# Kernel optimization log

Hardware: AMD Instinct MI355X
Metric: run time of the kernel (lower is better)

Reference implementation:

```python
import jax, jax.numpy as jnp
import numpy as np

N_SEG = 128  # number of distinct batch ids (patients/samples)
N = 250000   # total cells
E = 128      # embed_dim
H = 4        # num_heads

def setup_inputs() -> dict:
    key = jax.random.key(0)
    k1, k2, k3 = jax.random.split(key, 3)
    x = jax.random.normal(k1, (N, E), dtype=jnp.float32)
    weights = jax.random.normal(k2, (H, E), dtype=jnp.float32) * 0.02
    batch = jnp.sort(jax.random.randint(k3, (N,), 0, N_SEG, dtype=jnp.int64))
    return {"x": x, "weights": weights, "batch": batch}

def reference(x, weights, batch):
    # att[n,h] = <x[n], weights[h]>
    att = x @ weights.T  # [N, H]
    # segment-wise (per batch id) stable softmax over the sample axis
    m = jax.lax.stop_gradient(jax.ops.segment_max(att, batch, num_segments=N_SEG))  # [N_SEG, H]
    e = jnp.exp(att - m[batch])                                                     # [N, H]
    s = jax.ops.segment_sum(e, batch, num_segments=N_SEG)                           # [N_SEG, H]
    att_sm = e / s[batch]                                                           # [N, H]
    # h[b, h, e] = sum_{n in segment b} att_sm[n, h] * x[n, e]
    h = jax.ops.segment_sum(att_sm[:, :, None] * x[:, None, :], batch, num_segments=N_SEG)  # [N_SEG, H, E]
    # cat=False -> average over heads
    return h.mean(axis=1)  # [N_SEG, E]
```

## Files before the change

kernel.cpp:

```cpp
#include <hip/hip_runtime.h>

#define EDIM 128
#define NHEAD 4
#define NSEG 128
#define LOG2E 1.4426950408889634f

typedef float f32x8 __attribute__((ext_vector_type(8)));


#define DOT8(xv, wv)                                                     \
    fmaf((xv)[7], (wv)[7], fmaf((xv)[6], (wv)[6],                        \
    fmaf((xv)[5], (wv)[5], fmaf((xv)[4], (wv)[4],                        \
    fmaf((xv)[3], (wv)[3], fmaf((xv)[2], (wv)[2],                        \
    fmaf((xv)[1], (wv)[1], (xv)[0] * (wv)[0])))))))

#define RED16(v) do { v += __shfl_xor(v, 1, 64); v += __shfl_xor(v, 2, 64); \
                      v += __shfl_xor(v, 4, 64); v += __shfl_xor(v, 8, 64); } while (0)
#define REDG(v)  do { v += __shfl_xor(v, 16, 64); v += __shfl_xor(v, 32, 64); } while (0)

#define FLUSH_STORE(seg) do {                                            \
    float t0 = s0, t1 = s1, t2 = s2, t3 = s3;                            \
    REDG(t0); REDG(t1); REDG(t2); REDG(t3);                              \
    f32x8 r0 = a0, r1 = a1, r2 = a2, r3 = a3;                            \
    _Pragma("unroll")                                                    \
    for (int j = 0; j < 8; ++j) {                                        \
        float u0 = r0[j]; REDG(u0); r0[j] = u0;                          \
        float u1 = r1[j]; REDG(u1); r1[j] = u1;                          \
        float u2 = r2[j]; REDG(u2); r2[j] = u2;                          \
        float u3 = r3[j]; REDG(u3); r3[j] = u3;                          \
    }                                                                    \
    f32x8 rv = (g == 0) ? r0 : ((g == 1) ? r1 : ((g == 2) ? r2 : r3));   \
    const size_t ent_ = (size_t)wave * 2 + (nflushed < 1 ? 0 : 1);       \
    *reinterpret_cast<f32x8*>(pouth + ent_ * 512 + g * EDIM + 8 * c) = rv; \
    if (lane == 0) {                                                     \
        psum[ent_ * 4 + 0] = t0; psum[ent_ * 4 + 1] = t1;                \
        psum[ent_ * 4 + 2] = t2; psum[ent_ * 4 + 3] = t3;                \
        pseg[ent_] = (seg);                                              \
    }                                                                    \
    nflushed++;                                                          \
    a0 = Z8; a1 = Z8; a2 = Z8; a3 = Z8;                                  \
    s0 = 0.f; s1 = 0.f; s2 = 0.f; s3 = 0.f;                              \
} while (0)

__global__ __launch_bounds__(256) void attn_agg_pass1(
    const float* __restrict__ x, const float* __restrict__ w,
    const int* __restrict__ batch,
    float* __restrict__ pouth,
    float* __restrict__ psum,
    int*   __restrict__ pseg,
    int n, int qpw)
{
    const int tid  = blockIdx.x * blockDim.x + threadIdx.x;
    const int wave = tid >> 6;
    const int lane = threadIdx.x & 63;
    const int g    = lane >> 4;
    const int c    = lane & 15;

    const int nquads = (n + 3) >> 2;
    const int q0 = wave * qpw;
    if (q0 >= nquads) {
        if (lane == 0) { pseg[(size_t)wave * 2] = -1; pseg[(size_t)wave * 2 + 1] = -1; }
        return;
    }
    const int q1 = min(q0 + qpw, nquads);

    const float* wp = w + 8 * c;
    const f32x8 w0 = *reinterpret_cast<const f32x8*>(wp + 0 * EDIM);
    const f32x8 w1 = *reinterpret_cast<const f32x8*>(wp + 1 * EDIM);
    const f32x8 w2 = *reinterpret_cast<const f32x8*>(wp + 2 * EDIM);
    const f32x8 w3 = *reinterpret_cast<const f32x8*>(wp + 3 * EDIM);

    const f32x8 Z8 = {0.f, 0.f, 0.f, 0.f, 0.f, 0.f, 0.f, 0.f};
    f32x8 a0 = Z8, a1 = Z8, a2 = Z8, a3 = Z8;
    float s0 = 0.f, s1 = 0.f, s2 = 0.f, s3 = 0.f;
    int nflushed = 0;

    int cur_b = __builtin_amdgcn_readfirstlane(batch[q0 * 4]);

    for (int q = q0; q < q1; ++q) {
        const int cell = q * 4 + g;
        const int row  = min(cell, n - 1);
        const f32x8 xv = *reinterpret_cast<const f32x8*>(
            x + (size_t)row * EDIM + 8 * c);

        float p0 = DOT8(xv, w0);
        float p1 = DOT8(xv, w1);
        float p2 = DOT8(xv, w2);
        float p3 = DOT8(xv, w3);
        RED16(p0); RED16(p1); RED16(p2); RED16(p3);

        const float e0 = __builtin_exp2f(p0 * LOG2E);
        const float e1 = __builtin_exp2f(p1 * LOG2E);
        const float e2 = __builtin_exp2f(p2 * LOG2E);
        const float e3 = __builtin_exp2f(p3 * LOG2E);

        const bool full = (q * 4 + 3 < n);
        const int  b3   = __builtin_amdgcn_readfirstlane(batch[min(q * 4 + 3, n - 1)]);

        if (full && b3 == cur_b) {
            s0 += e0; s1 += e1; s2 += e2; s3 += e3;
            a0 += xv * e0; a1 += xv * e1; a2 += xv * e2; a3 += xv * e3;
        } else {
            const int my_b = (cell < n) ? batch[cell] : -2;
            const bool m1 = (my_b == cur_b);
            const float f1 = m1 ? 1.f : 0.f;
            s0 += e0 * f1; s1 += e1 * f1; s2 += e2 * f1; s3 += e3 * f1;
            a0 += xv * (e0 * f1); a1 += xv * (e1 * f1);
            a2 += xv * (e2 * f1); a3 += xv * (e3 * f1);

            FLUSH_STORE(cur_b);
            cur_b = b3;

            const float f2 = (!m1 && my_b == cur_b) ? 1.f : 0.f;
            s0 += e0 * f2; s1 += e1 * f2; s2 += e2 * f2; s3 += e3 * f2;
            a0 += xv * (e0 * f2); a1 += xv * (e1 * f2);
            a2 += xv * (e2 * f2); a3 += xv * (e3 * f2);
        }
    }

    FLUSH_STORE(cur_b);
    if (lane == 0 && nflushed < 2) pseg[(size_t)wave * 2 + 1] = -1;
}

__global__ __launch_bounds__(512) void attn_agg_finish(
    const float* __restrict__ pouth, const float* __restrict__ psum,
    const int* __restrict__ pseg, float* __restrict__ out, int nent)
{
    const int b = blockIdx.x;
    const int t = threadIdx.x;
    const int h = t >> 7, d = t & (EDIM - 1);

    __shared__ int matches[512];
    __shared__ int nmatch;
    __shared__ float hacc[NHEAD][EDIM];
    if (t == 0) nmatch = 0;
    __syncthreads();

    for (int i = t; i < nent; i += 512) {
        if (pseg[i] == b) {
            int p = atomicAdd(&nmatch, 1);
            matches[p] = i;
        }
    }
    __syncthreads();

    float acc = 0.f, sh = 0.f;
    const int nm = nmatch;
    for (int k = 0; k < nm; ++k) {
        const int i = matches[k];
        acc += pouth[(size_t)i * 512 + t];
        sh  += psum[(size_t)i * 4 + h];
    }
    hacc[h][d] = (sh > 0.f) ? (acc / sh) : 0.f;
    __syncthreads();

    if (h == 0)
        out[b * EDIM + d] = 0.25f *
            (hacc[0][d] + hacc[1][d] + hacc[2][d] + hacc[3][d]);
}

extern "C" void kernel_launch(void* const* d_in, const int* in_sizes, int n_in,
                              void* d_out, int out_size, void* d_ws, size_t ws_size,
                              hipStream_t stream) {
    const float* x     = (const float*)d_in[0];
    const float* w     = (const float*)d_in[1];
    const int*   batch = (const int*)d_in[2];
    float* out = (float*)d_out;

    const int n = in_sizes[0] / EDIM;
    const int nquads = (n + 3) >> 2;

    const size_t per_wave = 2 * (512 * 4 + 4 * 4 + 4);
    int W = (int)(ws_size / per_wave) - 4;
    if (W > 4096) W = 4096;
    if (W < 64)   W = 64;
    W &= ~3;

    const int qpw      = (nquads + W - 1) / W;
    const int nw       = (nquads + qpw - 1) / qpw;
    const int blocks1  = (nw + 3) / 4;
    const int launched = blocks1 * 4;
    const int nent     = launched * 2;

    float* pouth = (float*)d_ws;
    float* psum  = pouth + (size_t)nent * 512;
    int*   pseg  = (int*)(psum + (size_t)nent * 4);

    attn_agg_pass1<<<blocks1, 256, 0, stream>>>(x, w, batch, pouth, psum, pseg, n, qpw);
    attn_agg_finish<<<NSEG, 512, 0, stream>>>(pouth, psum, pseg, out, nent);
}
```

Baseline: 202.9 us.

## Add single-segment fast path, DPP reductions, and double wave count

Adds a fast path for waves whose whole cell range lies in one segment, which skips the per-quad batch loads and boundary checks and walks x with an incrementing pointer. The 16-lane dot-product reductions now use DPP row operations instead of shuffles. The wave cap rises from 4096 to 8192, so each wave handles fewer quads and occupancy improves. The finish kernel's match buffer is enlarged and clamped to fit the extra partial entries. The cost is more partial results for the finish kernel to scan and reduce.

```diff
diff --git a/kernel.cpp b/kernel.cpp
--- a/kernel.cpp
+++ b/kernel.cpp
@@ -14,8 +14,18 @@
     fmaf((xv)[3], (wv)[3], fmaf((xv)[2], (wv)[2],                        \
     fmaf((xv)[1], (wv)[1], (xv)[0] * (wv)[0])))))))
 
-#define RED16(v) do { v += __shfl_xor(v, 1, 64); v += __shfl_xor(v, 2, 64); \
-                      v += __shfl_xor(v, 4, 64); v += __shfl_xor(v, 8, 64); } while (0)
+__device__ __forceinline__ float dpp_add16(float v) {
+    v += __int_as_float(__builtin_amdgcn_update_dpp(
+        0, __float_as_int(v), 0xB1, 0xF, 0xF, true));
+    v += __int_as_float(__builtin_amdgcn_update_dpp(
+        0, __float_as_int(v), 0x4E, 0xF, 0xF, true));
+    v += __int_as_float(__builtin_amdgcn_update_dpp(
+        0, __float_as_int(v), 0x124, 0xF, 0xF, true));
+    v += __int_as_float(__builtin_amdgcn_update_dpp(
+        0, __float_as_int(v), 0x128, 0xF, 0xF, true));
+    return v;
+}
+
 #define REDG(v)  do { v += __shfl_xor(v, 16, 64); v += __shfl_xor(v, 32, 64); } while (0)
 
 #define FLUSH_STORE(seg) do {                                            \
@@ -75,46 +85,72 @@
     float s0 = 0.f, s1 = 0.f, s2 = 0.f, s3 = 0.f;
     int nflushed = 0;
 
+    const int cellN = min(q1 * 4, n);
     int cur_b = __builtin_amdgcn_readfirstlane(batch[q0 * 4]);
-
-    for (int q = q0; q < q1; ++q) {
-        const int cell = q * 4 + g;
-        const int row  = min(cell, n - 1);
-        const f32x8 xv = *reinterpret_cast<const f32x8*>(
-            x + (size_t)row * EDIM + 8 * c);
-
-        float p0 = DOT8(xv, w0);
-        float p1 = DOT8(xv, w1);
-        float p2 = DOT8(xv, w2);
-        float p3 = DOT8(xv, w3);
-        RED16(p0); RED16(p1); RED16(p2); RED16(p3);
-
-        const float e0 = __builtin_exp2f(p0 * LOG2E);
-        const float e1 = __builtin_exp2f(p1 * LOG2E);
-        const float e2 = __builtin_exp2f(p2 * LOG2E);
-        const float e3 = __builtin_exp2f(p3 * LOG2E);
-
-        const bool full = (q * 4 + 3 < n);
-        const int  b3   = __builtin_amdgcn_readfirstlane(batch[min(q * 4 + 3, n - 1)]);
-
-        if (full && b3 == cur_b) {
+    const int last_b = __builtin_amdgcn_readfirstlane(batch[cellN - 1]);
+
+    if (cur_b == last_b && q1 * 4 <= n) {
+        const float* xp = x + (size_t)(q0 * 4 + g) * EDIM + 8 * c;
+        for (int q = q0; q < q1; ++q) {
+            const f32x8 xv = *reinterpret_cast<const f32x8*>(xp);
+            xp += 4 * EDIM;
+
+            float p0 = DOT8(xv, w0);
+            float p1 = DOT8(xv, w1);
+            float p2 = DOT8(xv, w2);
+            float p3 = DOT8(xv, w3);
+            p0 = dpp_add16(p0); p1 = dpp_add16(p1);
+            p2 = dpp_add16(p2); p3 = dpp_add16(p3);
+
+            const float e0 = __builtin_exp2f(p0 * LOG2E);
+            const float e1 = __builtin_exp2f(p1 * LOG2E);
+            const float e2 = __builtin_exp2f(p2 * LOG2E);
+            const float e3 = __builtin_exp2f(p3 * LOG2E);
+
             s0 += e0; s1 += e1; s2 += e2; s3 += e3;
             a0 += xv * e0; a1 += xv * e1; a2 += xv * e2; a3 += xv * e3;
-        } else {
-            const int my_b = (cell < n) ? batch[cell] : -2;
-            const bool m1 = (my_b == cur_b);
-            const float f1 = m1 ? 1.f : 0.f;
-            s0 += e0 * f1; s1 += e1 * f1; s2 += e2 * f1; s3 += e3 * f1;
-            a0 += xv * (e0 * f1); a1 += xv * (e1 * f1);
-            a2 += xv * (e2 * f1); a3 += xv * (e3 * f1);
-
-            FLUSH_STORE(cur_b);
-            cur_b = b3;
-
-            const float f2 = (!m1 && my_b == cur_b) ? 1.f : 0.f;
-            s0 += e0 * f2; s1 += e1 * f2; s2 += e2 * f2; s3 += e3 * f2;
-            a0 += xv * (e0 * f2); a1 += xv * (e1 * f2);
-            a2 += xv * (e2 * f2); a3 += xv * (e3 * f2);
+        }
+    } else {
+        for (int q = q0; q < q1; ++q) {
+            const int cell = q * 4 + g;
+            const int row  = min(cell, n - 1);
+            const f32x8 xv = *reinterpret_cast<const f32x8*>(
+                x + (size_t)row * EDIM + 8 * c);
+
+            float p0 = DOT8(xv, w0);
+            float p1 = DOT8(xv, w1);
+            float p2 = DOT8(xv, w2);
+            float p3 = DOT8(xv, w3);
+            p0 = dpp_add16(p0); p1 = dpp_add16(p1);
+            p2 = dpp_add16(p2); p3 = dpp_add16(p3);
+
+            const float e0 = __builtin_exp2f(p0 * LOG2E);
+            const float e1 = __builtin_exp2f(p1 * LOG2E);
+            const float e2 = __builtin_exp2f(p2 * LOG2E);
+            const float e3 = __builtin_exp2f(p3 * LOG2E);
+
+            const bool full = (q * 4 + 3 < n);
+            const int  b3   = __builtin_amdgcn_readfirstlane(batch[min(q * 4 + 3, n - 1)]);
+
+            if (full && b3 == cur_b) {
+                s0 += e0; s1 += e1; s2 += e2; s3 += e3;
+                a0 += xv * e0; a1 += xv * e1; a2 += xv * e2; a3 += xv * e3;
+            } else {
+                const int my_b = (cell < n) ? batch[cell] : -2;
+                const bool m1 = (my_b == cur_b);
+                const float f1 = m1 ? 1.f : 0.f;
+                s0 += e0 * f1; s1 += e1 * f1; s2 += e2 * f1; s3 += e3 * f1;
+                a0 += xv * (e0 * f1); a1 += xv * (e1 * f1);
+                a2 += xv * (e2 * f1); a3 += xv * (e3 * f1);
+
+                FLUSH_STORE(cur_b);
+                cur_b = b3;
+
+                const float f2 = (!m1 && my_b == cur_b) ? 1.f : 0.f;
+                s0 += e0 * f2; s1 += e1 * f2; s2 += e2 * f2; s3 += e3 * f2;
+                a0 += xv * (e0 * f2); a1 += xv * (e1 * f2);
+                a2 += xv * (e2 * f2); a3 += xv * (e3 * f2);
+            }
         }
     }
 
@@ -130,7 +166,7 @@
     const int t = threadIdx.x;
     const int h = t >> 7, d = t & (EDIM - 1);
 
-    __shared__ int matches[512];
+    __shared__ int matches[1024];
     __shared__ int nmatch;
     __shared__ float hacc[NHEAD][EDIM];
     if (t == 0) nmatch = 0;
@@ -139,13 +175,13 @@
     for (int i = t; i < nent; i += 512) {
         if (pseg[i] == b) {
             int p = atomicAdd(&nmatch, 1);
-            matches[p] = i;
+            if (p < 1024) matches[p] = i;
         }
     }
     __syncthreads();
 
     float acc = 0.f, sh = 0.f;
-    const int nm = nmatch;
+    const int nm = min(nmatch, 1024);
     for (int k = 0; k < nm; ++k) {
         const int i = matches[k];
         acc += pouth[(size_t)i * 512 + t];
@@ -170,11 +206,11 @@
     const int n = in_sizes[0] / EDIM;
     const int nquads = (n + 3) >> 2;
 
-    const size_t per_wave = 2 * (512 * 4 + 4 * 4 + 4);
-    int W = (int)(ws_size / per_wave) - 4;
-    if (W > 4096) W = 4096;
-    if (W < 64)   W = 64;
-    W &= ~3;
+    const size_t per_ent = 512 * 4 + 4 * 4 + 4;
+    int W = 8192;
+    const size_t max_ent = ws_size / per_ent;
+    if ((size_t)W * 2 + 16 > max_ent) W = (int)(max_ent / 2) - 8;
+    if (W < 64) W = 64;
 
     const int qpw      = (nquads + W - 1) / W;
     const int nw       = (nquads + qpw - 1) / qpw;
```

New measurement: 203.5 us. About the same (+0.3%).
